# Performance work log

Measured on AMD Instinct MI355X. Metric: run time of the kernel, lower is better.

## Reference

```python
import jax, jax.numpy as jnp
import numpy as np

NINF = -1000000000.0
B, S, E = 2, 4096, 1024


def setup_inputs() -> dict:
    key = jax.random.key(0)
    ks = jax.random.split(key, 10)
    scale = 1.0 / np.sqrt(E)
    return {
        "query": jax.random.normal(ks[0], (B, S, E), dtype=jnp.float32),
        "key": jax.random.normal(ks[1], (B, S, E), dtype=jnp.float32),
        "value": jax.random.normal(ks[2], (B, S, E), dtype=jnp.float32),
        "mask": jax.random.randint(ks[3], (S, S), 0, 2).astype(bool),
        "Wq": jax.random.normal(ks[4], (E, E), dtype=jnp.float32) * scale,
        "bq": jnp.zeros((E,), dtype=jnp.float32),
        "Wk": jax.random.normal(ks[5], (E, E), dtype=jnp.float32) * scale,
        "bk": jnp.zeros((E,), dtype=jnp.float32),
        "Wv": jax.random.normal(ks[6], (E, E), dtype=jnp.float32) * scale,
        "bv": jnp.zeros((E,), dtype=jnp.float32),
    }


def reference(query, key, value, mask, Wq, bq, Wk, bk, Wv, bv):
    # linear projections (nn.Linear convention: x @ W.T + b)
    q = jnp.einsum('bse,fe->bsf', query, Wq) + bq   # [B,S,E]
    k = jnp.einsum('bse,fe->bsf', key, Wk) + bk
    v = jnp.einsum('bse,fe->bsf', value, Wv) + bv
    # full QK^T score matrix [B,S,S], scaled by sqrt(E) of projected query
    scores = jnp.einsum('bqe,bke->bqk', q, k) / jnp.sqrt(jnp.float32(E))
    scores = jnp.where(mask, jnp.float32(NINF), scores)  # True = ignored
    attn = jax.nn.softmax(scores, axis=-1)
    return jnp.einsum('bqk,bkv->bqv', attn, v)
```

## Files before the change

### kernel.cpp

```cpp
#include <hip/hip_runtime.h>
#include <hip/hip_bf16.h>


typedef _Float16 f16_t;
typedef _Float16 f16x8 __attribute__((ext_vector_type(8)));
typedef float f32x4 __attribute__((ext_vector_type(4)));
typedef unsigned long long u64;
typedef unsigned int uint;

union PackH8 { f16x8 v; f16_t e[8]; };

__device__ __forceinline__ f32x4 mfma_f16(f16x8 a, f16x8 b, f32x4 c) {
  return __builtin_amdgcn_mfma_f32_16x16x32_f16(a, b, c, 0, 0, 0);
}

__device__ __forceinline__ void cp16(const f16_t* g, f16_t* l) {
  __builtin_amdgcn_global_load_lds(
      (const __attribute__((address_space(1))) unsigned int*)g,
      (__attribute__((address_space(3))) unsigned int*)l, 16, 0, 0);
}

__global__ __launch_bounds__(256) void cvt_mask(
    const float* __restrict__ q, const float* __restrict__ k,
    const float* __restrict__ v, const float* __restrict__ wq,
    const float* __restrict__ wk, const float* __restrict__ wv,
    const int* __restrict__ mask,
    f16_t* __restrict__ xq, f16_t* __restrict__ xk, f16_t* __restrict__ xv,
    f16_t* __restrict__ wqh, f16_t* __restrict__ wkh, f16_t* __restrict__ wvh,
    u64* __restrict__ mb) {
  if (blockIdx.y == 6) {
    const int lane = threadIdx.x & 63;
    int wid = blockIdx.x * 4 + (threadIdx.x >> 6);
    for (int w = wid; w < 262144; w += 16384) {
      const int pred = mask[(size_t)w * 64 + lane] != 0;
      u64 b = __ballot(pred);
      if (lane == 0) mb[w] = b;
    }
    return;
  }
  const float* src; f16_t* dst; size_t n;
  switch (blockIdx.y) {
    case 0: src = q;  dst = xq;  n = 8388608; break;
    case 1: src = k;  dst = xk;  n = 8388608; break;
    case 2: src = v;  dst = xv;  n = 8388608; break;
    case 3: src = wq; dst = wqh; n = 1048576; break;
    case 4: src = wk; dst = wkh; n = 1048576; break;
    default: src = wv; dst = wvh; n = 1048576; break;
  }
  size_t i = ((size_t)blockIdx.x * 256 + threadIdx.x) * 8;
  if (i >= n) return;
  float4 a = *(const float4*)(src + i);
  float4 b = *(const float4*)(src + i + 4);
  PackH8 p;
  p.e[0] = (f16_t)a.x; p.e[1] = (f16_t)a.y; p.e[2] = (f16_t)a.z; p.e[3] = (f16_t)a.w;
  p.e[4] = (f16_t)b.x; p.e[5] = (f16_t)b.y; p.e[6] = (f16_t)b.z; p.e[7] = (f16_t)b.w;
  *(f16x8*)(dst + i) = p.v;
}

#define BARR { asm volatile("" ::: "memory"); __builtin_amdgcn_s_barrier(); }
#define VM0 asm volatile("s_waitcnt vmcnt(0)" ::: "memory");
#define VM3 asm volatile("s_waitcnt vmcnt(3)" ::: "memory");
#define VM4 asm volatile("s_waitcnt vmcnt(4)" ::: "memory");

__device__ __forceinline__ void core8ph(
    const f16_t* __restrict__ Ab, const f16_t* __restrict__ Bb,
    int m0, int n0, int K, int iters, f32x4 (&acc)[4][8]) {
  __shared__ f16_t lA[32768];
  __shared__ f16_t lB[32768];

  const int tid = threadIdx.x;
  const int w = tid >> 6, lane = tid & 63;
  const int quad = lane >> 4, l15 = lane & 15;
  const int wm = w >> 1, wn = w & 1;
  const int srow = lane >> 2;
  const int sg = (lane & 3) ^ ((lane >> 3) & 3);

  const uint aoff0 = (uint)(m0 + w * 32 + srow) * K + sg * 8;
  const uint aoff1 = aoff0 + 16 * K;
  const uint boff0 = (uint)(n0 + w * 32 + srow) * K + sg * 8;
  const uint boff1 = boff0 + 16 * K;
  const int ld0 = (w * 32) * 32;
  const int ld1 = (w * 32 + 16) * 32;

  int afo[4], bfo[8];
  const int swz = (quad ^ ((l15 >> 1) & 3)) * 8;
#pragma unroll
  for (int mi = 0; mi < 4; mi++) afo[mi] = (wm * 64 + mi * 16 + l15) * 32 + swz;
#pragma unroll
  for (int ni = 0; ni < 8; ni++) bfo[ni] = (wn * 128 + ni * 16 + l15) * 32 + swz;

#define STG_A(sl, kb) { cp16(Ab + aoff0 + (kb), lA + (sl) * 8192 + ld0); \
                        cp16(Ab + aoff1 + (kb), lA + (sl) * 8192 + ld1); }
#define STG_B(sl, kb) { cp16(Bb + boff0 + (kb), lB + (sl) * 8192 + ld0); \
                        cp16(Bb + boff1 + (kb), lB + (sl) * 8192 + ld1); }
#define RD_AF(dst, SL) { _Pragma("unroll") for (int mi = 0; mi < 4; mi++) \
      dst[mi] = *(const f16x8*)(lA + (SL) * 8192 + afo[mi]); }
#define RD_B03(dst, SL) { _Pragma("unroll") for (int ni = 0; ni < 4; ni++) \
      dst[ni] = *(const f16x8*)(lB + (SL) * 8192 + bfo[ni]); }
#define RD_B47(dst, SL) { _Pragma("unroll") for (int ni = 0; ni < 4; ni++) \
      dst[ni] = *(const f16x8*)(lB + (SL) * 8192 + bfo[ni + 4]); }
#define MM_Q0(ar, br) { __builtin_amdgcn_s_setprio(1); \
    _Pragma("unroll") for (int mi = 0; mi < 4; mi++) { \
      _Pragma("unroll") for (int nj = 0; nj < 4; nj++) \
        acc[mi][nj] = mfma_f16(ar[mi], br[nj], acc[mi][nj]); } \
    __builtin_amdgcn_s_setprio(0); }
#define MM_Q1(ar, br) { __builtin_amdgcn_s_setprio(1); \
    _Pragma("unroll") for (int mi = 0; mi < 4; mi++) { \
      _Pragma("unroll") for (int nj = 0; nj < 4; nj++) \
        acc[mi][4 + nj] = mfma_f16(ar[mi], br[nj], acc[mi][4 + nj]); } \
    __builtin_amdgcn_s_setprio(0); }

  f16x8 afA[4], afB[4], b0A[4], b0B[4], b47[4];

  STG_A(0, 0) STG_B(0, 0)
  STG_A(1, 32) STG_B(1, 32)
  STG_A(2, 64) STG_B(2, 64)
  VM4
  BARR
  RD_AF(afA, 0) RD_B03(b0A, 0)

  for (int i = 0; i < iters - 1; i++) {
    const int t0 = 2 * i;
    const int kb3 = (t0 + 1) * 64 + 32;
    const int kb0 = (t0 + 2) * 64;
    const int kb1 = kb0 + 32;
    const int kb2 = (t0 + 3) * 64;
     RD_B47(b47, 0) STG_A(3, kb3) MM_Q0(afA, b0A) VM4 BARR
     RD_AF(afB, 1) RD_B03(b0B, 1) STG_B(3, kb3) MM_Q1(afA, b47) BARR
     RD_B47(b47, 1) STG_A(0, kb0) MM_Q0(afB, b0B) VM4 BARR
     RD_AF(afA, 2) RD_B03(b0A, 2) STG_B(0, kb0) MM_Q1(afB, b47) BARR
     RD_B47(b47, 2) STG_A(1, kb1) MM_Q0(afA, b0A) VM4 BARR
     RD_AF(afB, 3) RD_B03(b0B, 3) STG_B(1, kb1) MM_Q1(afA, b47) BARR
     RD_B47(b47, 3) STG_A(2, kb2) MM_Q0(afB, b0B) VM4 BARR
     RD_AF(afA, 0) RD_B03(b0A, 0) STG_B(2, kb2) MM_Q1(afB, b47) BARR
  }
  {
    const int kbp = K - 32;
     RD_B47(b47, 0) STG_A(3, kbp) MM_Q0(afA, b0A) VM4 BARR
     RD_AF(afB, 1) RD_B03(b0B, 1) STG_B(3, kbp) MM_Q1(afA, b47) BARR
     RD_B47(b47, 1) MM_Q0(afB, b0B) VM4 BARR
     RD_AF(afA, 2) RD_B03(b0A, 2) MM_Q1(afB, b47) BARR
     RD_B47(b47, 2) MM_Q0(afA, b0A) VM0 BARR
     RD_AF(afB, 3) RD_B03(b0B, 3) MM_Q1(afA, b47) BARR
     RD_B47(b47, 3) MM_Q0(afB, b0B) BARR
     MM_Q1(afB, b47)
  }
#undef STG_A
#undef STG_B
#undef RD_AF
#undef RD_B03
#undef RD_B47
#undef MM_Q0
#undef MM_Q1
}

__device__ __forceinline__ void core4ph(
    const f16_t* __restrict__ Ab, const f16_t* __restrict__ Bb,
    int m0, int n0, int K, int iters, f32x4 (&acc)[4][4]) {
  __shared__ f16_t lA[32768];
  __shared__ f16_t lB[16384];

  const int tid = threadIdx.x;
  const int w = tid >> 6, lane = tid & 63;
  const int quad = lane >> 4, l15 = lane & 15;
  const int wm = w >> 1, wn = w & 1;
  const int sg = (lane & 3) ^ ((lane >> 3) & 3);

  const uint arow = (uint)(w * 16 + (lane >> 2));
  const uint aoff0 = (uint)(m0 + arow) * K + sg * 8;
  const uint aoff1 = aoff0 + 128 * K;
  const uint boff  = (uint)(n0 + arow) * K + sg * 8;
  const int ldw = w * 512;

  int afo[4], bfo[4];
  const int swz = (quad ^ ((l15 >> 1) & 3)) * 8;
#pragma unroll
  for (int mi = 0; mi < 4; mi++) afo[mi] = (wm * 64 + mi * 16 + l15) * 32 + swz;
#pragma unroll
  for (int ni = 0; ni < 4; ni++) bfo[ni] = (wn * 64 + ni * 16 + l15) * 32 + swz;

#define STG4(sl, kb) { cp16(Ab + aoff0 + (kb), lA + (sl) * 8192 + ldw); \
                       cp16(Ab + aoff1 + (kb), lA + (sl) * 8192 + 4096 + ldw); \
                       cp16(Bb + boff  + (kb), lB + (sl) * 4096 + ldw); }
#define RD4(adst, bdst, SL) { \
    _Pragma("unroll") for (int mi = 0; mi < 4; mi++) \
      adst[mi] = *(const f16x8*)(lA + (SL) * 8192 + afo[mi]); \
    _Pragma("unroll") for (int ni = 0; ni < 4; ni++) \
      bdst[ni] = *(const f16x8*)(lB + (SL) * 4096 + bfo[ni]); }
#define MM4(ar, br) { __builtin_amdgcn_s_setprio(1); \
    _Pragma("unroll") for (int mi = 0; mi < 4; mi++) { \
      _Pragma("unroll") for (int ni = 0; ni < 4; ni++) \
        acc[mi][ni] = mfma_f16(ar[mi], br[ni], acc[mi][ni]); } \
    __builtin_amdgcn_s_setprio(0); }

  f16x8 afA[4], afB[4], bfA[4], bfB[4];

  STG4(0, 0)
  STG4(1, 32)
  STG4(2, 64)
  VM3
  BARR
  RD4(afA, bfA, 0)

  for (int i = 0; i < iters - 1; i++) {
    const int t0 = 2 * i;
     RD4(afB, bfB, 1) STG4(3, (t0 + 1) * 64 + 32) MM4(afA, bfA) VM3 BARR
     RD4(afA, bfA, 2) STG4(0, (t0 + 2) * 64) MM4(afB, bfB) VM3 BARR
     RD4(afB, bfB, 3) STG4(1, (t0 + 2) * 64 + 32) MM4(afA, bfA) VM3 BARR
     RD4(afA, bfA, 0) STG4(2, (t0 + 3) * 64) MM4(afB, bfB) VM3 BARR
  }
  {
     RD4(afB, bfB, 1) STG4(3, K - 32) MM4(afA, bfA) VM3 BARR
     RD4(afA, bfA, 2) MM4(afB, bfB) VM0 BARR
     RD4(afB, bfB, 3) MM4(afA, bfA) BARR
     MM4(afB, bfB)
  }
#undef STG4
#undef RD4
#undef MM4
}

__global__ __launch_bounds__(512, 2) void gemm512(
    const f16_t* __restrict__ A, const f16_t* __restrict__ B,
    f16_t* __restrict__ C, const float* __restrict__ bias0,
    const float* __restrict__ bias1, int K,
    long sAz, long sBz, long sCz, float scale0, float scale1, int Cstride) {
  const int bz = blockIdx.z;
  const int n0 = blockIdx.x * 256;
  const int m0 = blockIdx.y * 256;
  const f16_t* Ab = A + (size_t)sAz * bz;
  const f16_t* Bb = B + (size_t)sBz * bz;

  f32x4 acc[4][8] = {};
  core8ph(Ab, Bb, m0, n0, K, K >> 7, acc);

  const int tid = threadIdx.x;
  const int w = tid >> 6, lane = tid & 63;
  const int quad = lane >> 4, l15 = lane & 15;
  const int wm = w >> 1, wn = w & 1;
  const float* bias = bz ? bias1 : bias0;
  const float scale = bz ? scale1 : scale0;
  f16_t* Cb = C + (size_t)sCz * bz;
#pragma unroll
  for (int mi = 0; mi < 4; mi++) {
#pragma unroll
    for (int ni = 0; ni < 8; ni++) {
      const int gm0 = m0 + wm * 64 + mi * 16 + quad * 4;
      const int gn = n0 + wn * 128 + ni * 16 + l15;
#pragma unroll
      for (int r = 0; r < 4; r++) {
        const int gm = gm0 + r;
        Cb[(size_t)gm * Cstride + gn] = (f16_t)((acc[mi][ni][r] + bias[gn]) * scale);
      }
    }
  }
}

__global__ __launch_bounds__(512, 2) void gemm256(
    const f16_t* __restrict__ A, const f16_t* __restrict__ B,
    f16_t* __restrict__ C, const float* __restrict__ bias0, int K) {
  const int n0 = blockIdx.x * 128;
  const int m0 = blockIdx.y * 256;

  f32x4 acc[4][4] = {};
  core4ph(A, B, m0, n0, K, K >> 7, acc);

  const int tid = threadIdx.x;
  const int w = tid >> 6, lane = tid & 63;
  const int quad = lane >> 4, l15 = lane & 15;
  const int wm = w >> 1, wn = w & 1;
#pragma unroll
  for (int mi = 0; mi < 4; mi++) {
#pragma unroll
    for (int ni = 0; ni < 4; ni++) {
      const int gm0 = m0 + wm * 64 + mi * 16 + quad * 4;
      const int gn = n0 + wn * 64 + ni * 16 + l15;
#pragma unroll
      for (int r = 0; r < 4; r++) {
        const int gm = gm0 + r;
        const int bb = gn >> 12;
        const int s = gn & 4095;
        C[(size_t)bb * 4194304 + (size_t)gm * 4096 + s] =
            (f16_t)(acc[mi][ni][r] + bias0[gm]);
      }
    }
  }
}

__global__ __launch_bounds__(512, 2) void gemm_qk(
    const f16_t* __restrict__ A, const f16_t* __restrict__ B,
    f16_t* __restrict__ S, const u64* __restrict__ mb,
    float* __restrict__ lrow) {
  const int bid = blockIdx.x;
  const int xcd = bid & 7;
  const int l = bid >> 3;
  const int bz = l >> 5;
  const int r5 = l & 31;
  const int m0 = (xcd * 2 + (r5 >> 4)) * 256;
  const int n0 = (r5 & 15) * 256;
  const f16_t* Ab = A + (size_t)4194304 * bz;
  const f16_t* Bb = B + (size_t)4194304 * bz;

  f32x4 acc[4][8] = {};
  core8ph(Ab, Bb, m0, n0, 1024, 8, acc);

  const int tid = threadIdx.x;
  const int w = tid >> 6, lane = tid & 63;
  const int quad = lane >> 4, l15 = lane & 15;
  const int wm = w >> 1, wn = w & 1;
  f16_t* Sb = S + (size_t)16777216 * bz;
  float* lb = lrow + bz * 4096;
  const int wbase = (n0 >> 6) + wn * 2;
#pragma unroll
  for (int mi = 0; mi < 4; mi++) {
#pragma unroll
    for (int r = 0; r < 4; r++) {
      const int gm = m0 + wm * 64 + mi * 16 + quad * 4 + r;
      const u64 w0 = mb[(size_t)gm * 64 + wbase];
      const u64 w1 = mb[(size_t)gm * 64 + wbase + 1];
      float rs = 0.f;
#pragma unroll
      for (int ni = 0; ni < 8; ni++) {
        const int col_l = ni * 16 + l15;
        const u64 mw = (ni < 4) ? w0 : w1;
        const int bit = (int)((mw >> (col_l & 63)) & 1);
        const float p = bit ? 0.f : __expf(acc[mi][ni][r] - 3.0f);
        Sb[(size_t)gm * 4096 + n0 + wn * 128 + col_l] = (f16_t)p;
        rs += p;
      }
      rs += __shfl_xor(rs, 1); rs += __shfl_xor(rs, 2);
      rs += __shfl_xor(rs, 4); rs += __shfl_xor(rs, 8);
      if (l15 == 0) atomicAdd(&lb[gm], rs);
    }
  }
}

__global__ __launch_bounds__(512, 2) void gemm_pv(
    const f16_t* __restrict__ S, const f16_t* __restrict__ V,
    float* __restrict__ O, const float* __restrict__ lrow) {
  const int bid = blockIdx.x;
  const int xcd = bid & 7;
  const int l = bid >> 3;
  const int bz = l >> 4;
  const int r4 = l & 15;
  const int m0 = (xcd * 2 + (r4 >> 3)) * 256;
  const int n0 = (r4 & 7) * 128;

  const f16_t* Ab = S + (size_t)16777216 * bz;
  const f16_t* Bb = V + (size_t)4194304 * bz;

  f32x4 acc[4][4] = {};
  core4ph(Ab, Bb, m0, n0, 4096, 32, acc);

  const int tid = threadIdx.x;
  const int w = tid >> 6, lane = tid & 63;
  const int quad = lane >> 4, l15 = lane & 15;
  const int wm = w >> 1, wn = w & 1;
  float* Ob = O + (size_t)4194304 * bz;
  const float* lb = lrow + bz * 4096;
#pragma unroll
  for (int mi = 0; mi < 4; mi++) {
#pragma unroll
    for (int ni = 0; ni < 4; ni++) {
      const int gm0 = m0 + wm * 64 + mi * 16 + quad * 4;
      const int gn = n0 + wn * 64 + ni * 16 + l15;
#pragma unroll
      for (int r = 0; r < 4; r++) {
        const int gm = gm0 + r;
        Ob[(size_t)gm * 1024 + gn] = acc[mi][ni][r] * (1.0f / lb[gm]);
      }
    }
  }
}

extern "C" void kernel_launch(void* const* d_in, const int* in_sizes, int n_in,
                              void* d_out, int out_size, void* d_ws, size_t ws_size,
                              hipStream_t stream) {
  const float* query = (const float*)d_in[0];
  const float* key_  = (const float*)d_in[1];
  const float* value = (const float*)d_in[2];
  const int* mask    = (const int*)d_in[3];
  const float* Wq = (const float*)d_in[4];
  const float* bq = (const float*)d_in[5];
  const float* Wk = (const float*)d_in[6];
  const float* bk = (const float*)d_in[7];
  const float* Wv = (const float*)d_in[8];
  const float* bv = (const float*)d_in[9];
  float* out = (float*)d_out;

  const size_t MB = (size_t)1 << 20;
  char* w = (char*)d_ws;
  f16_t* qb  = (f16_t*)(w);
  f16_t* kb  = (f16_t*)(w + 16 * MB);
  f16_t* vt  = (f16_t*)(w + 32 * MB);
  f16_t* xq  = (f16_t*)(w + 48 * MB);
  f16_t* xk  = (f16_t*)(w + 64 * MB);
  f16_t* xv  = (f16_t*)(w + 80 * MB);
  f16_t* wqh = (f16_t*)(w + 96 * MB);
  f16_t* wkh = (f16_t*)(w + 98 * MB);
  f16_t* wvh = (f16_t*)(w + 100 * MB);
  f16_t* S   = (f16_t*)(w + 48 * MB);
  float* ls  = (float*)(w + 112 * MB);
  u64* mb = (u64*)d_out;

  cvt_mask<<<dim3(4096, 7), 256, 0, stream>>>(query, key_, value, Wq, Wk, Wv,
                                              mask, xq, xk, xv, wqh, wkh, wvh, mb);
  gemm512<<<dim3(4, 32, 2), 512, 0, stream>>>(
      xq, wqh, qb, bq, bk, 1024, 8388608L, 1048576L, 8388608L,
      0.03125f, 1.0f, 1024);
  gemm256<<<dim3(64, 4), 512, 0, stream>>>(wvh, xv, vt, bv, 1024);
  hipMemsetAsync(ls, 0, 2 * 4096 * sizeof(float), stream);
  gemm_qk<<<dim3(512), 512, 0, stream>>>(qb, kb, S, mb, ls);
  gemm_pv<<<dim3(256), 512, 0, stream>>>(S, vt, out, ls);
}
```

Measured before the change: 436.6 us.

## Retile PV GEMM to 128x128 blocks with inline LDS loop; compact conversion grid

Measured after the change: 436.8 us. About the same (+0.0%).

```diff
diff --git a/kernel.cpp b/kernel.cpp
--- a/kernel.cpp
+++ b/kernel.cpp
@@ -28,9 +28,10 @@
     f16_t* __restrict__ xq, f16_t* __restrict__ xk, f16_t* __restrict__ xv,
     f16_t* __restrict__ wqh, f16_t* __restrict__ wkh, f16_t* __restrict__ wvh,
     u64* __restrict__ mb) {
-  if (blockIdx.y == 6) {
+  const int bid = blockIdx.x;
+  if (bid >= 13824) {
     const int lane = threadIdx.x & 63;
-    int wid = blockIdx.x * 4 + (threadIdx.x >> 6);
+    int wid = (bid - 13824) * 4 + (threadIdx.x >> 6);
     for (int w = wid; w < 262144; w += 16384) {
       const int pred = mask[(size_t)w * 64 + lane] != 0;
       u64 b = __ballot(pred);
@@ -38,17 +39,23 @@
     }
     return;
   }
-  const float* src; f16_t* dst; size_t n;
-  switch (blockIdx.y) {
-    case 0: src = q;  dst = xq;  n = 8388608; break;
-    case 1: src = k;  dst = xk;  n = 8388608; break;
-    case 2: src = v;  dst = xv;  n = 8388608; break;
-    case 3: src = wq; dst = wqh; n = 1048576; break;
-    case 4: src = wk; dst = wkh; n = 1048576; break;
-    default: src = wv; dst = wvh; n = 1048576; break;
-  }
-  size_t i = ((size_t)blockIdx.x * 256 + threadIdx.x) * 8;
-  if (i >= n) return;
+  const float* src; f16_t* dst; int rb;
+  if (bid < 12288) {
+    rb = bid & 4095;
+    switch (bid >> 12) {
+      case 0: src = q; dst = xq; break;
+      case 1: src = k; dst = xk; break;
+      default: src = v; dst = xv; break;
+    }
+  } else {
+    rb = (bid - 12288) & 511;
+    switch ((bid - 12288) >> 9) {
+      case 0: src = wq; dst = wqh; break;
+      case 1: src = wk; dst = wkh; break;
+      default: src = wv; dst = wvh; break;
+    }
+  }
+  size_t i = ((size_t)rb * 256 + threadIdx.x) * 8;
   float4 a = *(const float4*)(src + i);
   float4 b = *(const float4*)(src + i + 4);
   PackH8 p;
@@ -335,27 +342,70 @@
   }
 }
 
-__global__ __launch_bounds__(512, 2) void gemm_pv(
+__global__ __launch_bounds__(256, 2) void gemm_pv(
     const f16_t* __restrict__ S, const f16_t* __restrict__ V,
     float* __restrict__ O, const float* __restrict__ lrow) {
+  __shared__ f16_t sA[8192];
+  __shared__ f16_t sB[8192];
   const int bid = blockIdx.x;
   const int xcd = bid & 7;
   const int l = bid >> 3;
-  const int bz = l >> 4;
-  const int r4 = l & 15;
-  const int m0 = (xcd * 2 + (r4 >> 3)) * 256;
-  const int n0 = (r4 & 7) * 128;
-
+  const int bz = l >> 5;
+  const int r = l & 31;
+  const int m0 = (xcd * 4 + (r >> 3)) * 128;
+  const int n0 = (r & 7) * 128;
   const f16_t* Ab = S + (size_t)16777216 * bz;
   const f16_t* Bb = V + (size_t)4194304 * bz;
 
+  const int tid = threadIdx.x;
+  const int w = tid >> 6, lane = tid & 63;
+  const int quad = lane >> 4, l15 = lane & 15;
+  const int wm = w >> 1, wn = w & 1;
+
+  const int srow = lane >> 3;
+  const int sg = (lane & 7) ^ srow;
+
+  int ar[4][2], br[4][2];
+#pragma unroll
+  for (int mi = 0; mi < 4; mi++)
+#pragma unroll
+    for (int ks = 0; ks < 2; ks++) {
+      ar[mi][ks] = (wm * 64 + mi * 16 + l15) * 64 +
+                   (((ks << 2) + quad) ^ (l15 & 7)) * 8;
+      br[mi][ks] = (wn * 64 + mi * 16 + l15) * 64 +
+                   (((ks << 2) + quad) ^ (l15 & 7)) * 8;
+    }
+
   f32x4 acc[4][4] = {};
-  core4ph(Ab, Bb, m0, n0, 4096, 32, acc);
-
-  const int tid = threadIdx.x;
-  const int w = tid >> 6, lane = tid & 63;
-  const int quad = lane >> 4, l15 = lane & 15;
-  const int wm = w >> 1, wn = w & 1;
+
+  for (int k0 = 0; k0 < 4096; k0 += 64) {
+    __syncthreads();
+#pragma unroll
+    for (int j = 0; j < 4; j++) {
+      const int c = j * 4 + w;
+      cp16(Ab + (uint)(m0 + c * 8 + srow) * 4096 + sg * 8 + k0, sA + c * 512);
+      cp16(Bb + (uint)(n0 + c * 8 + srow) * 4096 + sg * 8 + k0, sB + c * 512);
+    }
+    VM0
+    __syncthreads();
+#pragma unroll
+    for (int ks = 0; ks < 2; ks++) {
+      f16x8 af[4], bf[4];
+#pragma unroll
+      for (int mi = 0; mi < 4; mi++) {
+        af[mi] = *(const f16x8*)(sA + ar[mi][ks]);
+        bf[mi] = *(const f16x8*)(sB + br[mi][ks]);
+      }
+      __builtin_amdgcn_s_setprio(1);
+#pragma unroll
+      for (int mi = 0; mi < 4; mi++)
+#pragma unroll
+        for (int ni = 0; ni < 4; ni++)
+          acc[mi][ni] = mfma_f16(af[mi], bf[ni], acc[mi][ni]);
+      __builtin_amdgcn_s_setprio(0);
+    }
+  }
+
   float* Ob = O + (size_t)4194304 * bz;
   const float* lb = lrow + bz * 4096;
 #pragma unroll
@@ -365,9 +415,9 @@
       const int gm0 = m0 + wm * 64 + mi * 16 + quad * 4;
       const int gn = n0 + wn * 64 + ni * 16 + l15;
 #pragma unroll
-      for (int r = 0; r < 4; r++) {
-        const int gm = gm0 + r;
-        Ob[(size_t)gm * 1024 + gn] = acc[mi][ni][r] * (1.0f / lb[gm]);
+      for (int r2 = 0; r2 < 4; r2++) {
+        const int gm = gm0 + r2;
+        Ob[(size_t)gm * 1024 + gn] = acc[mi][ni][r2] * (1.0f / lb[gm]);
       }
     }
   }
@@ -403,13 +453,13 @@
   float* ls  = (float*)(w + 112 * MB);
   u64* mb = (u64*)d_out;
 
-  cvt_mask<<<dim3(4096, 7), 256, 0, stream>>>(query, key_, value, Wq, Wk, Wv,
-                                              mask, xq, xk, xv, wqh, wkh, wvh, mb);
+  cvt_mask<<<dim3(17920), 256, 0, stream>>>(query, key_, value, Wq, Wk, Wv,
+                                            mask, xq, xk, xv, wqh, wkh, wvh, mb);
   gemm512<<<dim3(4, 32, 2), 512, 0, stream>>>(
       xq, wqh, qb, bq, bk, 1024, 8388608L, 1048576L, 8388608L,
       0.03125f, 1.0f, 1024);
   gemm256<<<dim3(64, 4), 512, 0, stream>>>(wvh, xv, vt, bv, 1024);
   hipMemsetAsync(ls, 0, 2 * 4096 * sizeof(float), stream);
   gemm_qk<<<dim3(512), 512, 0, stream>>>(qb, kb, S, mb, ls);
-  gemm_pv<<<dim3(256), 512, 0, stream>>>(S, vt, out, ls);
-}
+  gemm_pv<<<dim3(512), 256, 0, stream>>>(S, vt, out, ls);
+}
```
